# Performance work log

Hardware: AMD Instinct MI355X
Metric: run time of the kernel (lower is better)

## Reference

```python
import math
import jax, jax.numpy as jnp
import numpy as np

N_HEADS = 16
D_EMBED = 1024
D_HEAD = D_EMBED // N_HEADS  # 64; only used for the scale factor (see bug note)
B, N = 4, 4096


def setup_inputs() -> dict:
    key = jax.random.key(0)
    k1, k2, k3, k4, k5 = jax.random.split(key, 5)
    return {
        "x": jax.random.normal(k1, (B, N, D_EMBED), dtype=jnp.float32),
        "W_qkv_w": jax.random.normal(k2, (3 * D_EMBED, D_EMBED), dtype=jnp.float32) * 0.02,
        "W_qkv_b": jax.random.normal(k3, (3 * D_EMBED,), dtype=jnp.float32) * 0.02,
        "W_o_w": jax.random.normal(k4, (D_EMBED, D_EMBED), dtype=jnp.float32) * 0.02,
        "W_o_b": jax.random.normal(k5, (D_EMBED,), dtype=jnp.float32) * 0.02,
    }


def reference(x, W_qkv_w, W_qkv_b, W_o_w, W_o_b):
    # Faithful to source, including its bugs:
    #  - q/k/v are never actually reshaped to heads (the .view().transpose()
    #    results are discarded), so attention runs over full d_embed vectors
    #    with scale 1/sqrt(d_head).
    #  - the final transpose(1,2).reshape scrambles the output layout.
    b, n, d = x.shape
    qkv = x @ W_qkv_w.T + W_qkv_b                      # [b, n, 3d]
    q, k, v = jnp.split(qkv, 3, axis=-1)               # each [b, n, d]
    scores = jnp.einsum("bqd,bkd->bqk", q, k)          # [b, n, n]
    causal = jnp.triu(jnp.ones((n, n), dtype=bool), 1)
    scale = jnp.float32(1.0 / math.sqrt(D_HEAD))
    scores = jnp.where(causal, -jnp.inf, scores * scale)
    weights = jax.nn.softmax(scores, axis=-1)
    out = jnp.einsum("bqk,bkd->bqd", weights, v)       # [b, n, d]
    out = jnp.swapaxes(out, 1, 2).reshape(b, n, d)     # scramble (as in source)
    return out @ W_o_w.T + W_o_b
```

## Files before the change

### kernel.cpp

```cpp
#include <hip/hip_runtime.h>
#include <math.h>

#define TB 256

typedef __attribute__((ext_vector_type(8))) short short8_t;
typedef __attribute__((ext_vector_type(4))) float f32x4;

__device__ __forceinline__ ushort f2bf(float f) {
    uint u = __float_as_uint(f);
    return (ushort)((u + 0x7FFFu + ((u >> 16) & 1u)) >> 16);
}

__device__ __forceinline__ void gload_lds16(const void* g, void* l) {
    __builtin_amdgcn_global_load_lds(
        (const __attribute__((address_space(1))) void*)g,
        (__attribute__((address_space(3))) void*)l, 16, 0, 0);
}

template<int EPI, bool TRI, bool KLIM, bool REVX>
__global__ __launch_bounds__(TB)
void gemm_bf16(const ushort* __restrict__ A, int lda,
               const ushort* __restrict__ B, int ldb,
               const float* __restrict__ bias,
               void* __restrict__ Cv, int ldc,
               int K, float alpha, int off)
{
    constexpr int BM = 128, BN = 128, BK = 32;
    const int m0 = blockIdx.y * BM;
    const int nb = REVX ? (gridDim.x - 1 - blockIdx.x) : blockIdx.x;
    const int n0 = nb * BN;
    if (TRI && n0 > m0 + off + BM - 1) return;

    const int tid = threadIdx.x;
    const int lane = tid & 63;
    const int wid = tid >> 6;
    const int wr = wid >> 1, wc = wid & 1;

    __shared__ __align__(16) ushort As[3][BM * BK];
    __shared__ __align__(16) ushort Bs[3][BN * BK];

    f32x4 acc[4][4];
    const f32x4 zero = {0.f, 0.f, 0.f, 0.f};
    #pragma unroll
    for (int mi = 0; mi < 4; mi++)
        #pragma unroll
        for (int ni = 0; ni < 4; ni++) acc[mi][ni] = zero;

    const int klim = KLIM ? (n0 + off + BN) : K;
    const int kend = klim < K ? klim : K;
    const int nt = kend / BK;

    auto STAGE = [&](int t, int s) {
        const int k0 = t * BK;
        const int c = wid * 2;
        const int row0 = c * 16 + (lane >> 2);
        const int row1 = row0 + 16;
        const int kh = (lane & 3) * 8;
        gload_lds16(&A[(size_t)(m0 + row0) * lda + k0 + kh], (char*)&As[s][0] + c * 1024);
        gload_lds16(&A[(size_t)(m0 + row1) * lda + k0 + kh], (char*)&As[s][0] + (c + 1) * 1024);
        gload_lds16(&B[(size_t)(n0 + row0) * ldb + k0 + kh], (char*)&Bs[s][0] + c * 1024);
        gload_lds16(&B[(size_t)(n0 + row1) * ldb + k0 + kh], (char*)&Bs[s][0] + (c + 1) * 1024);
    };

    STAGE(0, 0);
    if (nt > 1) {
        STAGE(1, 1);
        asm volatile("s_waitcnt vmcnt(4)" ::: "memory");
    } else {
        asm volatile("s_waitcnt vmcnt(0)" ::: "memory");
    }
    __builtin_amdgcn_s_barrier();

    for (int t = 0; t < nt; t++) {
        const int cur = t % 3;
        if (t + 2 < nt) STAGE(t + 2, (t + 2) % 3);

        const int frow = lane & 15;
        const int kh8  = (lane >> 4) * 8;
        short8_t a[4], b[4];
        #pragma unroll
        for (int mi = 0; mi < 4; mi++)
            a[mi] = *(const short8_t*)&As[cur][(wr * 64 + mi * 16 + frow) * BK + kh8];
        #pragma unroll
        for (int ni = 0; ni < 4; ni++)
            b[ni] = *(const short8_t*)&Bs[cur][(wc * 64 + ni * 16 + frow) * BK + kh8];
        #pragma unroll
        for (int mi = 0; mi < 4; mi++)
            #pragma unroll
            for (int ni = 0; ni < 4; ni++)
                acc[mi][ni] = __builtin_amdgcn_mfma_f32_16x16x32_bf16(
                    a[mi], b[ni], acc[mi][ni], 0, 0, 0);

        if (t + 1 < nt) {
            if (t + 2 < nt) asm volatile("s_waitcnt vmcnt(4)" ::: "memory");
            else            asm volatile("s_waitcnt vmcnt(0)" ::: "memory");
            __builtin_amdgcn_s_barrier();
        }
    }

    const int col = lane & 15;
    const int rb  = (lane >> 4) * 4;
    #pragma unroll
    for (int mi = 0; mi < 4; mi++) {
        #pragma unroll
        for (int ni = 0; ni < 4; ni++) {
            const int r = m0 + wr * 64 + mi * 16 + rb;
            const int c = n0 + wc * 64 + ni * 16 + col;
            f32x4 v = acc[mi][ni];
            if (EPI == 0) {
                ushort* C = (ushort*)Cv;
                const float bz = bias[c];
                #pragma unroll
                for (int t = 0; t < 4; t++)
                    C[(size_t)(r + t) * ldc + c] = f2bf(v[t] + bz);
            } else if (EPI == 1) {
                float* C = (float*)Cv;
                #pragma unroll
                for (int t = 0; t < 4; t++)
                    C[(size_t)(r + t) * ldc + c] = v[t] * alpha;
            } else if (EPI == 2) {
                ushort* C = (ushort*)Cv;
                #pragma unroll
                for (int t = 0; t < 4; t++)
                    C[(size_t)(r + t) * ldc + c + off] = f2bf(v[t]);
            } else {
                float* C = (float*)Cv;
                const float bz = bias[c];
                #pragma unroll
                for (int t = 0; t < 4; t++)
                    C[(size_t)(r + t) * ldc + c] = v[t] + bz;
            }
        }
    }
}

__global__ __launch_bounds__(TB)
void conv_f32_bf16(const float* __restrict__ in, ushort* __restrict__ out, int n4)
{
    for (int i = blockIdx.x * TB + threadIdx.x; i < n4; i += gridDim.x * TB) {
        float4 v = ((const float4*)in)[i];
        ushort4 o;
        o.x = f2bf(v.x); o.y = f2bf(v.y); o.z = f2bf(v.z); o.w = f2bf(v.w);
        ((ushort4*)out)[i] = o;
    }
}

__global__ __launch_bounds__(TB)
void transposeV(const ushort* __restrict__ V, int ldv, ushort* __restrict__ Vt)
{
    __shared__ ushort Ls[64][65];
    const int n0 = blockIdx.x * 64, d0 = blockIdx.y * 64;
    const int t = threadIdx.x;
    #pragma unroll
    for (int p = 0; p < 4; p++) {
        const int row = p * 16 + (t >> 4);
        const int c4 = (t & 15) * 4;
        ushort4 v = *(const ushort4*)&V[(size_t)(n0 + row) * ldv + d0 + c4];
        Ls[row][c4 + 0] = v.x; Ls[row][c4 + 1] = v.y;
        Ls[row][c4 + 2] = v.z; Ls[row][c4 + 3] = v.w;
    }
    __syncthreads();
    #pragma unroll
    for (int p = 0; p < 4; p++) {
        const int d = p * 16 + (t >> 4);
        const int n4 = (t & 15) * 4;
        ushort4 o;
        o.x = Ls[n4 + 0][d]; o.y = Ls[n4 + 1][d];
        o.z = Ls[n4 + 2][d]; o.w = Ls[n4 + 3][d];
        *(ushort4*)&Vt[(size_t)(d0 + d) * 4096 + n0 + n4] = o;
    }
}

__global__ __launch_bounds__(TB)
void softmax_prefix(float* __restrict__ Sp, ushort* __restrict__ Pp, int r0)
{
    const int local = blockIdx.x;
    const int r = r0 + local;
    const int pe = ((r >> 7) << 7) + 128;
    float* p = Sp + (size_t)local * 4096;
    ushort* q = Pp + (size_t)local * 4096;
    const int t = threadIdx.x;
    const int wv = t >> 6, ln = t & 63;
    __shared__ float red[4];

    float lm = -INFINITY;
    for (int k4 = t * 4; k4 < pe; k4 += 1024) {
        float4 v = *(const float4*)&p[k4];
        lm = (k4 + 0 <= r) ? fmaxf(lm, v.x) : lm;
        lm = (k4 + 1 <= r) ? fmaxf(lm, v.y) : lm;
        lm = (k4 + 2 <= r) ? fmaxf(lm, v.z) : lm;
        lm = (k4 + 3 <= r) ? fmaxf(lm, v.w) : lm;
    }
    #pragma unroll
    for (int m = 1; m < 64; m <<= 1) lm = fmaxf(lm, __shfl_xor(lm, m, 64));
    if (ln == 0) red[wv] = lm;
    __syncthreads();
    const float mx = fmaxf(fmaxf(red[0], red[1]), fmaxf(red[2], red[3]));
    __syncthreads();

    float ls = 0.f;
    for (int k4 = t * 4; k4 < pe; k4 += 1024) {
        float4 v = *(const float4*)&p[k4];
        float4 e;
        e.x = (k4 + 0 <= r) ? __expf(v.x - mx) : 0.f;
        e.y = (k4 + 1 <= r) ? __expf(v.y - mx) : 0.f;
        e.z = (k4 + 2 <= r) ? __expf(v.z - mx) : 0.f;
        e.w = (k4 + 3 <= r) ? __expf(v.w - mx) : 0.f;
        ls += e.x + e.y + e.z + e.w;
        *(float4*)&p[k4] = e;
    }
    #pragma unroll
    for (int m = 1; m < 64; m <<= 1) ls += __shfl_xor(ls, m, 64);
    if (ln == 0) red[wv] = ls;
    __syncthreads();
    const float inv = 1.0f / (red[0] + red[1] + red[2] + red[3]);
    for (int k4 = t * 4; k4 < pe; k4 += 1024) {
        float4 e = *(const float4*)&p[k4];
        ushort4 o;
        o.x = f2bf(e.x * inv); o.y = f2bf(e.y * inv);
        o.z = f2bf(e.z * inv); o.w = f2bf(e.w * inv);
        *(ushort4*)&q[k4] = o;
    }
}

extern "C" void kernel_launch(void* const* d_in, const int* in_sizes, int n_in,
                              void* d_out, int out_size, void* d_ws, size_t ws_size,
                              hipStream_t stream)
{
    const float* x    = (const float*)d_in[0];
    const float* Wqkv = (const float*)d_in[1];
    const float* bqkv = (const float*)d_in[2];
    const float* Wo   = (const float*)d_in[3];
    const float* bo   = (const float*)d_in[4];
    float* out = (float*)d_out;

    ushort* xbf  = (ushort*)d_ws;
    ushort* Wq   = xbf  + (size_t)4 * 4096 * 1024;
    ushort* Wob  = Wq   + (size_t)3072 * 1024;
    ushort* qkvb = Wob  + (size_t)1024 * 1024;
    ushort* Vtb  = qkvb + (size_t)4096 * 3072;
    ushort* Tall = Vtb  + (size_t)1024 * 4096;
    ushort* Pch  = Tall + (size_t)4 * 4096 * 1024;
    const size_t fixedB = ((size_t)4 * 4096 * 1024 + (size_t)3072 * 1024 +
                           (size_t)1024 * 1024 + (size_t)4096 * 3072 +
                           (size_t)1024 * 4096 + (size_t)4 * 4096 * 1024) * 2;
    int CH = 4096;
    while (CH > 128 && fixedB + (size_t)CH * 4096 * 6 > ws_size) CH >>= 1;
    float* Sch = (float*)(Pch + (size_t)CH * 4096);

    dim3 blk(TB);

    conv_f32_bf16<<<2048, blk, 0, stream>>>(x,    xbf, 4 * 4096 * 1024 / 4);
    conv_f32_bf16<<<256,  blk, 0, stream>>>(Wqkv, Wq,  3072 * 1024 / 4);
    conv_f32_bf16<<<128,  blk, 0, stream>>>(Wo,   Wob, 1024 * 1024 / 4);

    for (int b = 0; b < 4; b++) {
        const ushort* xb = xbf + (size_t)b * 4096 * 1024;
        gemm_bf16<0, false, false, false><<<dim3(24, 32), blk, 0, stream>>>(
            xb, 1024, Wq, 1024, bqkv, qkvb, 3072, 1024, 1.f, 0);

        transposeV<<<dim3(64, 16), blk, 0, stream>>>(qkvb + 2048, 3072, Vtb);

        for (int r0 = 0; r0 < 4096; r0 += CH) {
            gemm_bf16<1, true, false, false><<<dim3(32, CH / 128), blk, 0, stream>>>(
                qkvb + (size_t)r0 * 3072, 3072, qkvb + 1024, 3072, nullptr,
                Sch, 4096, 1024, 0.125f, r0);
            softmax_prefix<<<dim3(CH), blk, 0, stream>>>(Sch, Pch, r0);
            gemm_bf16<2, false, true, true><<<dim3(CH / 128, 8), blk, 0, stream>>>(
                Vtb, 4096, Pch, 4096, nullptr,
                Tall + (size_t)b * 4096 * 1024, 4096, 4096, 1.f, r0);
        }
    }

    gemm_bf16<3, false, false, false><<<dim3(8, 128), blk, 0, stream>>>(
        Tall, 1024, Wob, 1024, bo, out, 1024, 1024, 1.f, 0);
}
```

Measured before the change: 860.1 us.

## Fuse x conversion into QKV GEMM and split-K the PV GEMM

The QKV GEMM now reads fp32 x directly and converts it to bf16 while staging A tiles into LDS, which drops the separate x conversion pass and its bf16 buffer. The P·V GEMM is split along K into two halves across blockIdx.z, and each half writes fp32 partials that a new reduce kernel sums into bf16. The fixed CH chunking is removed, so a full 4096-row score buffer is always assumed. This raises parallelism in the triangular-K PV GEMM at the cost of extra partial-sum traffic, a non-async A load path, and a larger workspace requirement.

```diff
diff --git a/kernel.cpp b/kernel.cpp
--- a/kernel.cpp
+++ b/kernel.cpp
@@ -17,9 +17,9 @@
         (__attribute__((address_space(3))) void*)l, 16, 0, 0);
 }
 
-template<int EPI, bool TRI, bool KLIM, bool REVX>
-__global__ __launch_bounds__(TB)
-void gemm_bf16(const ushort* __restrict__ A, int lda,
+template<int CONV, int EPI, bool TRI, bool KLIM, bool REVX, bool SPLITK>
+__global__ __launch_bounds__(TB)
+void gemm_bf16(const void* __restrict__ Av, int lda,
                const ushort* __restrict__ B, int ldb,
                const float* __restrict__ bias,
                void* __restrict__ Cv, int ldc,
@@ -48,35 +48,76 @@
 
     const int klim = KLIM ? (n0 + off + BN) : K;
     const int kend = klim < K ? klim : K;
-    const int nt = kend / BK;
+    const int ntf = kend / BK;
+    int t0 = 0, t1 = ntf;
+    if (SPLITK) {
+        const int half = (ntf + 1) >> 1;
+        if (blockIdx.z == 0) t1 = half; else t0 = half;
+    }
+    const int ntl = t1 - t0;
 
     auto STAGE = [&](int t, int s) {
         const int k0 = t * BK;
+        if (CONV) {
+            const float* Af = (const float*)Av;
+            #pragma unroll
+            for (int h = 0; h < 2; h++) {
+                const int q = tid + h * TB;
+                const int row = q >> 2;
+                const int kp = (q & 3) * 8;
+                const float* src = &Af[(size_t)(m0 + row) * lda + k0 + kp];
+                float4 u0 = *(const float4*)src;
+                float4 u1 = *(const float4*)(src + 4);
+                short8_t sv;
+                sv[0] = (short)f2bf(u0.x); sv[1] = (short)f2bf(u0.y);
+                sv[2] = (short)f2bf(u0.z); sv[3] = (short)f2bf(u0.w);
+                sv[4] = (short)f2bf(u1.x); sv[5] = (short)f2bf(u1.y);
+                sv[6] = (short)f2bf(u1.z); sv[7] = (short)f2bf(u1.w);
+                *(short8_t*)&As[s][row * BK + kp] = sv;
+            }
+        } else {
+            const ushort* Ab = (const ushort*)Av;
+            const int c = wid * 2;
+            const int row0 = c * 16 + (lane >> 2);
+            const int row1 = row0 + 16;
+            const int kh = (lane & 3) * 8;
+            gload_lds16(&Ab[(size_t)(m0 + row0) * lda + k0 + kh],
+                        (char*)&As[s][0] + c * 1024);
+            gload_lds16(&Ab[(size_t)(m0 + row1) * lda + k0 + kh],
+                        (char*)&As[s][0] + (c + 1) * 1024);
+        }
         const int c = wid * 2;
         const int row0 = c * 16 + (lane >> 2);
         const int row1 = row0 + 16;
         const int kh = (lane & 3) * 8;
-        gload_lds16(&A[(size_t)(m0 + row0) * lda + k0 + kh], (char*)&As[s][0] + c * 1024);
-        gload_lds16(&A[(size_t)(m0 + row1) * lda + k0 + kh], (char*)&As[s][0] + (c + 1) * 1024);
-        gload_lds16(&B[(size_t)(n0 + row0) * ldb + k0 + kh], (char*)&Bs[s][0] + c * 1024);
-        gload_lds16(&B[(size_t)(n0 + row1) * ldb + k0 + kh], (char*)&Bs[s][0] + (c + 1) * 1024);
+        gload_lds16(&B[(size_t)(n0 + row0) * ldb + k0 + kh],
+                    (char*)&Bs[s][0] + c * 1024);
+        gload_lds16(&B[(size_t)(n0 + row1) * ldb + k0 + kh],
+                    (char*)&Bs[s][0] + (c + 1) * 1024);
     };
 
-    STAGE(0, 0);
-    if (nt > 1) {
-        STAGE(1, 1);
-        asm volatile("s_waitcnt vmcnt(4)" ::: "memory");
-    } else {
-        asm volatile("s_waitcnt vmcnt(0)" ::: "memory");
-    }
+    auto wait_pipe = [&]() {
+        if constexpr (CONV != 0) asm volatile("s_waitcnt vmcnt(2)" ::: "memory");
+        else                     asm volatile("s_waitcnt vmcnt(4)" ::: "memory");
+    };
+    auto wait_zero = [&]() { asm volatile("s_waitcnt vmcnt(0)" ::: "memory"); };
+    auto wait_lgkm = [&]() {
+        if constexpr (CONV != 0) asm volatile("s_waitcnt lgkmcnt(0)" ::: "memory");
+    };
+
+    STAGE(t0, 0);
+    if (ntl > 1) { STAGE(t0 + 1, 1); wait_pipe(); }
+    else         { wait_zero(); }
+    wait_lgkm();
     __builtin_amdgcn_s_barrier();
 
-    for (int t = 0; t < nt; t++) {
-        const int cur = t % 3;
-        if (t + 2 < nt) STAGE(t + 2, (t + 2) % 3);
-
-        const int frow = lane & 15;
-        const int kh8  = (lane >> 4) * 8;
+    const int frow = lane & 15;
+    const int kh8  = (lane >> 4) * 8;
+
+    for (int u = 0; u < ntl; u++) {
+        const int cur = u % 3;
+        if (u + 2 < ntl) STAGE(t0 + u + 2, (u + 2) % 3);
+
         short8_t a[4], b[4];
         #pragma unroll
         for (int mi = 0; mi < 4; mi++)
@@ -91,13 +132,17 @@
                 acc[mi][ni] = __builtin_amdgcn_mfma_f32_16x16x32_bf16(
                     a[mi], b[ni], acc[mi][ni], 0, 0, 0);
 
-        if (t + 1 < nt) {
-            if (t + 2 < nt) asm volatile("s_waitcnt vmcnt(4)" ::: "memory");
-            else            asm volatile("s_waitcnt vmcnt(0)" ::: "memory");
+        if (u + 1 < ntl) {
+            if (u + 2 < ntl) wait_pipe();
+            else             wait_zero();
+            wait_lgkm();
             __builtin_amdgcn_s_barrier();
         }
     }
 
+    void* Czv = Cv;
+    if (SPLITK)
+        Czv = (void*)((float*)Cv + (size_t)blockIdx.z * 1024 * 4096);
     const int col = lane & 15;
     const int rb  = (lane >> 4) * 4;
     #pragma unroll
@@ -108,23 +153,18 @@
             const int c = n0 + wc * 64 + ni * 16 + col;
             f32x4 v = acc[mi][ni];
             if (EPI == 0) {
-                ushort* C = (ushort*)Cv;
+                ushort* C = (ushort*)Czv;
                 const float bz = bias[c];
                 #pragma unroll
                 for (int t = 0; t < 4; t++)
                     C[(size_t)(r + t) * ldc + c] = f2bf(v[t] + bz);
             } else if (EPI == 1) {
-                float* C = (float*)Cv;
+                float* C = (float*)Czv;
                 #pragma unroll
                 for (int t = 0; t < 4; t++)
                     C[(size_t)(r + t) * ldc + c] = v[t] * alpha;
-            } else if (EPI == 2) {
-                ushort* C = (ushort*)Cv;
-                #pragma unroll
-                for (int t = 0; t < 4; t++)
-                    C[(size_t)(r + t) * ldc + c + off] = f2bf(v[t]);
             } else {
-                float* C = (float*)Cv;
+                float* C = (float*)Czv;
                 const float bz = bias[c];
                 #pragma unroll
                 for (int t = 0; t < 4; t++)
@@ -142,6 +182,20 @@
         ushort4 o;
         o.x = f2bf(v.x); o.y = f2bf(v.y); o.z = f2bf(v.z); o.w = f2bf(v.w);
         ((ushort4*)out)[i] = o;
+    }
+}
+
+__global__ __launch_bounds__(TB)
+void reduce_pair_bf16(const float* __restrict__ a, const float* __restrict__ b,
+                      ushort* __restrict__ o, int n4)
+{
+    for (int i = blockIdx.x * TB + threadIdx.x; i < n4; i += gridDim.x * TB) {
+        float4 x = ((const float4*)a)[i];
+        float4 y = ((const float4*)b)[i];
+        ushort4 z;
+        z.x = f2bf(x.x + y.x); z.y = f2bf(x.y + y.y);
+        z.z = f2bf(x.z + y.z); z.w = f2bf(x.w + y.w);
+        ((ushort4*)o)[i] = z;
     }
 }
 
@@ -234,44 +288,40 @@
     const float* bo   = (const float*)d_in[4];
     float* out = (float*)d_out;
 
-    ushort* xbf  = (ushort*)d_ws;
-    ushort* Wq   = xbf  + (size_t)4 * 4096 * 1024;
-    ushort* Wob  = Wq   + (size_t)3072 * 1024;
-    ushort* qkvb = Wob  + (size_t)1024 * 1024;
-    ushort* Vtb  = qkvb + (size_t)4096 * 3072;
-    ushort* Tall = Vtb  + (size_t)1024 * 4096;
-    ushort* Pch  = Tall + (size_t)4 * 4096 * 1024;
-    const size_t fixedB = ((size_t)4 * 4096 * 1024 + (size_t)3072 * 1024 +
-                           (size_t)1024 * 1024 + (size_t)4096 * 3072 +
-                           (size_t)1024 * 4096 + (size_t)4 * 4096 * 1024) * 2;
-    int CH = 4096;
-    while (CH > 128 && fixedB + (size_t)CH * 4096 * 6 > ws_size) CH >>= 1;
-    float* Sch = (float*)(Pch + (size_t)CH * 4096);
+    ushort* Wq    = (ushort*)d_ws;
+    ushort* Wob   = Wq    + (size_t)3072 * 1024;
+    ushort* qkvb  = Wob   + (size_t)1024 * 1024;
+    ushort* Vtb   = qkvb  + (size_t)4096 * 3072;
+    ushort* Tall  = Vtb   + (size_t)1024 * 4096;
+    ushort* Pch   = Tall  + (size_t)4 * 1024 * 4096;
+    float*  Sch   = (float*)(Pch + (size_t)4096 * 4096);
+    float*  Tpart = Sch + (size_t)4096 * 4096;
 
     dim3 blk(TB);
 
-    conv_f32_bf16<<<2048, blk, 0, stream>>>(x,    xbf, 4 * 4096 * 1024 / 4);
-    conv_f32_bf16<<<256,  blk, 0, stream>>>(Wqkv, Wq,  3072 * 1024 / 4);
-    conv_f32_bf16<<<128,  blk, 0, stream>>>(Wo,   Wob, 1024 * 1024 / 4);
+    conv_f32_bf16<<<256, blk, 0, stream>>>(Wqkv, Wq,  3072 * 1024 / 4);
+    conv_f32_bf16<<<128, blk, 0, stream>>>(Wo,   Wob, 1024 * 1024 / 4);
 
     for (int b = 0; b < 4; b++) {
-        const ushort* xb = xbf + (size_t)b * 4096 * 1024;
-        gemm_bf16<0, false, false, false><<<dim3(24, 32), blk, 0, stream>>>(
+        const float* xb = x + (size_t)b * 4096 * 1024;
+        gemm_bf16<1, 0, false, false, false, false><<<dim3(24, 32), blk, 0, stream>>>(
             xb, 1024, Wq, 1024, bqkv, qkvb, 3072, 1024, 1.f, 0);
 
         transposeV<<<dim3(64, 16), blk, 0, stream>>>(qkvb + 2048, 3072, Vtb);
 
-        for (int r0 = 0; r0 < 4096; r0 += CH) {
-            gemm_bf16<1, true, false, false><<<dim3(32, CH / 128), blk, 0, stream>>>(
-                qkvb + (size_t)r0 * 3072, 3072, qkvb + 1024, 3072, nullptr,
-                Sch, 4096, 1024, 0.125f, r0);
-            softmax_prefix<<<dim3(CH), blk, 0, stream>>>(Sch, Pch, r0);
-            gemm_bf16<2, false, true, true><<<dim3(CH / 128, 8), blk, 0, stream>>>(
-                Vtb, 4096, Pch, 4096, nullptr,
-                Tall + (size_t)b * 4096 * 1024, 4096, 4096, 1.f, r0);
-        }
-    }
-
-    gemm_bf16<3, false, false, false><<<dim3(8, 128), blk, 0, stream>>>(
+        gemm_bf16<0, 1, true, false, false, false><<<dim3(32, 32), blk, 0, stream>>>(
+            qkvb, 3072, qkvb + 1024, 3072, nullptr, Sch, 4096, 1024, 0.125f, 0);
+
+        softmax_prefix<<<dim3(4096), blk, 0, stream>>>(Sch, Pch, 0);
+
+        gemm_bf16<0, 1, false, true, true, true><<<dim3(32, 8, 2), blk, 0, stream>>>(
+            Vtb, 4096, Pch, 4096, nullptr, Tpart, 4096, 4096, 1.f, 0);
+
+        reduce_pair_bf16<<<1024, blk, 0, stream>>>(
+            Tpart, Tpart + (size_t)1024 * 4096,
+            Tall + (size_t)b * 1024 * 4096, 1024 * 4096 / 4);
+    }
+
+    gemm_bf16<0, 3, false, false, false, false><<<dim3(8, 128), blk, 0, stream>>>(
         Tall, 1024, Wob, 1024, bo, out, 1024, 1024, 1.f, 0);
 }
```

Result: no change. 852.8 us (-0.8%).
